# Performance work log

Measured on AMD Instinct MI355X. Metric: run time of the kernel, lower is better.

Reference implementation:

```python
import jax, jax.numpy as jnp
import numpy as np
from functools import partial

VOCAB, EMB, HID, B, T, K = 30000, 256, 512, 128, 256, 12
START, STOP = 10, 11


def lstm_scan(xs, mask, W_ih, W_hh, b_ih, b_hh, h0, c0):
    """xs: [T,B,E], mask: [T,B] bool. PyTorch gate order i,f,g,o. Masked steps carry state (packed-seq semantics)."""
    def step(carry, inp):
        h, c = carry
        x_t, m_t = inp
        gates = x_t @ W_ih.T + h @ W_hh.T + (b_ih + b_hh)  # [B,4H]
        i, f, g, o = jnp.split(gates, 4, axis=-1)
        c_new = jax.nn.sigmoid(f) * c + jax.nn.sigmoid(i) * jnp.tanh(g)
        h_new = jax.nn.sigmoid(o) * jnp.tanh(c_new)
        m = m_t[:, None]
        h = jnp.where(m, h_new, h)
        c = jnp.where(m, c_new, c)
        return (h, c), h
    _, hs = jax.lax.scan(step, (h0, c0), (xs, mask))
    return hs  # [T,B,H]


def crf_log_partition(emissions, mask, trans):
    """emissions: [T,B,K], mask: [T,B]. Vectorized log-sum-exp forward algorithm."""
    b, k = emissions.shape[1], emissions.shape[2]
    alpha0 = jnp.full((b, k), -10000.0, emissions.dtype).at[:, START].set(0.0)
    def step(alpha, inp):
        emit_t, m_t = inp
        # alpha_new[b,j] = logsumexp_i(alpha[b,i] + trans[j,i]) + emit[b,j]
        scores = alpha[:, None, :] + trans[None, :, :]  # [B,Knext,Kprev]
        alpha_new = jax.nn.logsumexp(scores, axis=-1) + emit_t
        return jnp.where(m_t[:, None], alpha_new, alpha), None
    alpha, _ = jax.lax.scan(step, alpha0, (emissions, mask))
    return jax.nn.logsumexp(alpha + trans[STOP][None, :], axis=-1)  # [B]


def crf_gold_score(emissions_bt, tags, lengths, trans):
    """emissions_bt: [B,T,K]. Gold path score with <start> prepended and <stop> transition."""
    b, t = tags.shape
    tags_ext = jnp.concatenate([jnp.full((b, 1), START, tags.dtype), tags], axis=1)  # [B,T+1]
    prev, nxt = tags_ext[:, :-1], tags_ext[:, 1:]  # [B,T]
    trans_s = trans[nxt, prev]  # [B,T]
    emit_s = jnp.take_along_axis(emissions_bt, nxt[:, :, None], axis=2)[:, :, 0]  # [B,T]
    valid = jnp.arange(t)[None, :] < lengths[:, None]  # [B,T]
    score = jnp.sum(jnp.where(valid, trans_s + emit_s, 0.0), axis=1)
    last_tag = jnp.take_along_axis(tags, (lengths - 1)[:, None], axis=1)[:, 0]
    return score + trans[STOP, last_tag]


def setup_inputs() -> dict:
    key = jax.random.key(0)
    ks = jax.random.split(key, 16)
    s = 0.1
    x = jax.random.randint(ks[0], (B, T), 0, VOCAB)
    lengths = jax.random.randint(ks[1], (B,), 1, T + 1)
    tags = jax.random.randint(ks[2], (B, T), 0, K - 2)  # real labels only
    embedding = jax.random.normal(ks[3], (VOCAB, EMB), jnp.float32) * s
    W_ih_f = jax.random.normal(ks[4], (4 * HID, EMB), jnp.float32) * s
    W_hh_f = jax.random.normal(ks[5], (4 * HID, HID), jnp.float32) * s
    b_ih_f = jax.random.normal(ks[6], (4 * HID,), jnp.float32) * s
    b_hh_f = jax.random.normal(ks[7], (4 * HID,), jnp.float32) * s
    W_ih_b = jax.random.normal(ks[8], (4 * HID, EMB), jnp.float32) * s
    W_hh_b = jax.random.normal(ks[9], (4 * HID, HID), jnp.float32) * s
    b_ih_b = jax.random.normal(ks[10], (4 * HID,), jnp.float32) * s
    b_hh_b = jax.random.normal(ks[11], (4 * HID,), jnp.float32) * s
    fc_W = jax.random.normal(ks[12], (K, 2 * HID), jnp.float32) * s
    fc_b = jnp.zeros((K,), jnp.float32)
    trans = jax.random.normal(ks[13], (K, K), jnp.float32) * s
    trans = trans.at[START, :].set(-10000.0).at[:, STOP].set(-10000.0)
    h0 = jax.random.normal(ks[14], (2, B, HID), jnp.float32) * s
    c0 = jax.random.normal(ks[15], (2, B, HID), jnp.float32) * s
    return dict(x=x, lengths=lengths, tags=tags, embedding=embedding,
                W_ih_f=W_ih_f, W_hh_f=W_hh_f, b_ih_f=b_ih_f, b_hh_f=b_hh_f,
                W_ih_b=W_ih_b, W_hh_b=W_hh_b, b_ih_b=b_ih_b, b_hh_b=b_hh_b,
                fc_W=fc_W, fc_b=fc_b, trans=trans, h0=h0, c0=c0)


def reference(x, lengths, tags, embedding, W_ih_f, W_hh_f, b_ih_f, b_hh_f,
              W_ih_b, W_hh_b, b_ih_b, b_hh_b, fc_W, fc_b, trans, h0, c0):
    # neg_log_likelihood: BiLSTM emission feats -> CRF logZ - gold score. Dropout = eval (identity).
    emb = embedding[x]                 # [B,T,E]
    xs = emb.transpose(1, 0, 2)        # [T,B,E] time-major
    t = xs.shape[0]
    mask = jnp.arange(t)[:, None] < lengths[None, :]  # [T,B]
    hs_f = lstm_scan(xs, mask, W_ih_f, W_hh_f, b_ih_f, b_hh_f, h0[0], c0[0])
    hs_b = lstm_scan(xs[::-1], mask[::-1], W_ih_b, W_hh_b, b_ih_b, b_hh_b, h0[1], c0[1])[::-1]
    out = jnp.concatenate([hs_f, hs_b], axis=-1)      # [T,B,2H]
    emissions = out @ fc_W.T + fc_b                    # [T,B,K]
    log_z = crf_log_partition(emissions, mask, trans)  # [B]
    gold = crf_gold_score(emissions.transpose(1, 0, 2), tags, lengths, trans)  # [B]
    return log_z - gold  # per-sentence NLL, [B]
```

## Files before the change

kernel.cpp:

```cpp
#include <hip/hip_runtime.h>
#include <hip/hip_bf16.h>

#define TT 256
#define BB 128
#define EMBD 256
#define HID 512
#define KTAG 12
#define START_TAG 10
#define STOP_TAG 11
#define SMEM_BYTES 148608

typedef __attribute__((ext_vector_type(8))) short short8;
typedef __attribute__((ext_vector_type(4))) float f32x4;

__device__ __forceinline__ unsigned short f2bf(float f) {
    union { float f; unsigned int u; } v; v.f = f;
    unsigned int r = v.u + 0x7fffu + ((v.u >> 16) & 1u);
    return (unsigned short)(r >> 16);
}
__device__ __forceinline__ float fsig(float x) {
    return __fdividef(1.0f, 1.0f + __expf(-x));
}
__device__ __forceinline__ float ftanh(float x) {
    return 2.0f * __fdividef(1.0f, 1.0f + __expf(-2.0f * x)) - 1.0f;
}
__device__ __forceinline__ void gll16(const void* g, void* l) {
    __builtin_amdgcn_global_load_lds((const __attribute__((address_space(1))) void*)g,
                                     (__attribute__((address_space(3))) void*)l, 16, 0, 0);
}
__device__ __forceinline__ void pack8(const float* src, unsigned short* dst) {
    float4 v0 = *(const float4*)src;
    float4 v1 = *(const float4*)(src + 4);
    unsigned short tmp[8];
    tmp[0] = f2bf(v0.x); tmp[1] = f2bf(v0.y); tmp[2] = f2bf(v0.z); tmp[3] = f2bf(v0.w);
    tmp[4] = f2bf(v1.x); tmp[5] = f2bf(v1.y); tmp[6] = f2bf(v1.z); tmp[7] = f2bf(v1.w);
    *(uint4*)dst = *(const uint4*)tmp;
}

__global__ void prologue(const int* __restrict__ x, const float* __restrict__ emb,
                         const float* __restrict__ Wihf, const float* __restrict__ Whhf,
                         const float* __restrict__ Wihb, const float* __restrict__ Whhb,
                         const float* __restrict__ h0,
                         const float* __restrict__ bihf, const float* __restrict__ bhhf,
                         const float* __restrict__ bihb, const float* __restrict__ bhhb,
                         const float* __restrict__ fcW,
                         unsigned short* __restrict__ xs, unsigned short* __restrict__ Wr,
                         unsigned short* __restrict__ h0buf, float* __restrict__ bias2,
                         unsigned short* __restrict__ fcWr, unsigned int* __restrict__ ctrl)
{
    int blk = blockIdx.x;
    int tid = threadIdx.x;
    if (blk < 4096) {
        int i = blk * 256 + tid;
        int chk = i & 31;
        int row = i >> 5;
        int b = row & (BB - 1);
        int t = row >> 7;
        pack8(emb + (size_t)x[b * TT + t] * EMBD + chk * 8, xs + (size_t)row * EMBD + chk * 8);
    } else if (blk < 5632) {
        int i = (blk - 4096) * 256 + tid;
        int c8 = i % 96;
        int r2 = i / 96;
        int nr = r2 & 2047;
        int dir = r2 >> 11;
        int utile = nr >> 6;
        int r6 = nr & 63;
        int wm = r6 >> 4;
        int rr = r6 & 15;
        int ul = rr >> 2, g = rr & 3;
        int orow = g * HID + utile * 16 + wm * 4 + ul;
        int k0 = c8 * 8;
        const float* Wih = dir ? Wihb : Wihf;
        const float* Whh = dir ? Whhb : Whhf;
        const float* src = (k0 < EMBD) ? (Wih + (size_t)orow * EMBD + k0)
                                       : (Whh + (size_t)orow * HID + (k0 - EMBD));
        pack8(src, Wr + ((size_t)dir * 2048 + nr) * 768 + k0);
    } else {
        int i = (blk - 5632) * 256 + tid;
        if (i < 2 * BB * HID) h0buf[i] = f2bf(h0[i]);
        if (i < 2 * 2048) {
            int dir = i >> 11, j = i & 2047;
            bias2[i] = dir ? (bihb[j] + bhhb[j]) : (bihf[j] + bhhf[j]);
        }
        if (i < 16 * 1024) {
            int tag = i >> 10, k = i & 1023;
            fcWr[i] = f2bf(tag < KTAG ? fcW[tag * 1024 + k] : 0.0f);
        }
        if (i < 512) ctrl[i] = 0u;
    }
}

__launch_bounds__(256, 1)
__global__ void lstm_persistent(
    const unsigned short* __restrict__ xs, const unsigned short* __restrict__ Wr,
    const float* __restrict__ bias2, const int* __restrict__ lengths,
    const unsigned short* __restrict__ h0buf, const float* __restrict__ c0,
    unsigned short* __restrict__ hsf, unsigned short* __restrict__ hsb,
    unsigned int* __restrict__ ctrl)
{
    extern __shared__ char smem[];
    unsigned short* Wlds = (unsigned short*)smem;
    unsigned short* Abuf = (unsigned short*)(smem + 98304);
    unsigned short* hrep = (unsigned short*)(smem + 147456);

    const int blk = blockIdx.x;
    const int grp = blk & 7;
    const int dir = grp >> 2;
    const int btile = grp & 3;
    const int utile = blk >> 3;
    const int bg0 = btile * 32;

    const int tid = threadIdx.x;
    const int w = tid >> 6;
    const int l = tid & 63;
    const int l15 = l & 15, l16 = l >> 4;

    unsigned int* gflags = ctrl + 64 + grp * 32;

    unsigned short* hs = dir ? hsb : hsf;
    unsigned int* hs_u32 = (unsigned int*)hs;

    {
        const unsigned short* src0 =
            Wr + ((size_t)(dir * 2048 + utile * 64) + (w * 16 + l15)) * 768 + l16 * 8;
        #pragma unroll
        for (int ks = 0; ks < 24; ks++)
            gll16(src0 + ks * 32, Wlds + (w * 24 + ks) * 512);
    }

    const int u = utile * 16 + w * 4 + l16;
    const int bA = bg0 + l15, bB = bg0 + 16 + l15;
    const int lenA = lengths[bA], lenB = lengths[bB];
    float cA = c0[((size_t)dir * BB + bA) * HID + u];
    float cB = c0[((size_t)dir * BB + bB) * HID + u];
    float bias_r[4];
    #pragma unroll
    for (int g = 0; g < 4; g++) bias_r[g] = bias2[dir * 2048 + g * 512 + u];

    for (int s = 0; s < TT; s++) {
        const int t = dir ? (TT - 1 - s) : s;

        {
            int mm = w & 1, ksb = (w >> 1) * 4;
            const unsigned short* asrc =
                xs + ((size_t)t * BB + (bg0 + mm * 16 + l15)) * EMBD + l16 * 8;
            #pragma unroll
            for (int q = 0; q < 4; q++)
                gll16(asrc + (ksb + q) * 32, Abuf + (mm * 24 + ksb + q) * 512);
        }
        __syncthreads();

        f32x4 aA0 = {0.f,0.f,0.f,0.f}, aA1 = {0.f,0.f,0.f,0.f};
        f32x4 aB0 = {0.f,0.f,0.f,0.f}, aB1 = {0.f,0.f,0.f,0.f};
        auto mstep = [&](int ks, f32x4& xA, f32x4& xB) {
            short8 a  = *(const short8*)(Wlds + ((w * 24 + ks) << 9) + (l << 3));
            short8 b0 = *(const short8*)(Abuf + (ks << 9) + (l << 3));
            short8 b1 = *(const short8*)(Abuf + ((24 + ks) << 9) + (l << 3));
            xA = __builtin_amdgcn_mfma_f32_16x16x32_bf16(a, b0, xA, 0, 0, 0);
            xB = __builtin_amdgcn_mfma_f32_16x16x32_bf16(a, b1, xB, 0, 0, 0);
        };
        #pragma unroll
        for (int ks = 0; ks < 8; ks += 2) { mstep(ks, aA0, aB0); mstep(ks + 1, aA1, aB1); }

        if (s > 0) {
            if (tid < 64) {
                unsigned tgt = (unsigned)s;
                unsigned fidx = (unsigned)tid & 31u;
                while (true) {
                    unsigned v = __hip_atomic_load(&gflags[fidx], __ATOMIC_RELAXED,
                                                   __HIP_MEMORY_SCOPE_AGENT);
                    if (__all(v >= tgt)) break;
                }
            }
            __syncthreads();
        }
        const unsigned short* hsrc = (s == 0)
            ? (h0buf + (size_t)dir * BB * HID)
            : (hs + (size_t)(dir ? (t + 1) : (t - 1)) * BB * HID);

        {
            int mm = w & 1, ksb = 8 + (w >> 1) * 8;
            const unsigned short* asrcH = hsrc + (size_t)(bg0 + mm * 16 + l15) * HID + l16 * 8;
            #pragma unroll
            for (int q = 0; q < 8; q++)
                gll16(asrcH + ((ksb + q) * 32 - 256), Abuf + (mm * 24 + ksb + q) * 512);
        }
        __syncthreads();

        #pragma unroll
        for (int ks = 8; ks < 24; ks += 2) { mstep(ks, aA0, aB0); mstep(ks + 1, aA1, aB1); }
        f32x4 accA = aA0 + aA1;
        f32x4 accB = aB0 + aB1;

        {
            const int ksn = 8 + (u >> 5), kin = u & 31;
            const int baseA = ksn * 512 + ((kin >> 3) * 16 + l15) * 8 + (kin & 7);
            const int baseB = (24 + ksn) * 512 + ((kin >> 3) * 16 + l15) * 8 + (kin & 7);
            float giA = accA[0] + bias_r[0], gfA = accA[1] + bias_r[1];
            float ggA = accA[2] + bias_r[2], goA = accA[3] + bias_r[3];
            float cnA = fsig(gfA) * cA + fsig(giA) * ftanh(ggA);
            float hnA = fsig(goA) * ftanh(cnA);
            float giB = accB[0] + bias_r[0], gfB = accB[1] + bias_r[1];
            float ggB = accB[2] + bias_r[2], goB = accB[3] + bias_r[3];
            float cnB = fsig(gfB) * cB + fsig(giB) * ftanh(ggB);
            float hnB = fsig(goB) * ftanh(cnB);
            bool mA = t < lenA, mB = t < lenB;
            unsigned short hvA = mA ? f2bf(hnA) : Abuf[baseA];
            unsigned short hvB = mB ? f2bf(hnB) : Abuf[baseB];
            cA = mA ? cnA : cA;
            cB = mB ? cnB : cB;
            hrep[l15 * 18 + w * 4 + l16]        = hvA;
            hrep[(16 + l15) * 18 + w * 4 + l16] = hvB;
        }
        __syncthreads();

        {
            int bl = tid >> 3, up = tid & 7;
            unsigned v0 = hrep[bl * 18 + up * 2];
            unsigned v1 = hrep[bl * 18 + up * 2 + 1];
            unsigned pk = v0 | (v1 << 16);
            size_t widx = (((size_t)t * BB + (bg0 + bl)) * HID + utile * 16 + up * 2) >> 1;
            __hip_atomic_store(hs_u32 + widx, pk, __ATOMIC_RELAXED, __HIP_MEMORY_SCOPE_AGENT);
        }
        __syncthreads();

        if (tid == 0)
            __hip_atomic_store(&gflags[utile], (unsigned)(s + 1), __ATOMIC_RELAXED,
                               __HIP_MEMORY_SCOPE_AGENT);
    }
}

__global__ void emissions_mfma(const unsigned short* __restrict__ hsf,
                               const unsigned short* __restrict__ hsb,
                               const unsigned short* __restrict__ fcWr,
                               const float* __restrict__ fcb, float* __restrict__ emis)
{
    int wid = (blockIdx.x * blockDim.x + threadIdx.x) >> 6;
    int l = threadIdx.x & 63;
    int l15 = l & 15, l16 = l >> 4;
    int rowbase = wid * 16;
    f32x4 acc0 = {0.f,0.f,0.f,0.f}, acc1 = {0.f,0.f,0.f,0.f};
    auto estep = [&](const unsigned short* hsp, int ks, f32x4& acc) {
        short8 av = *(const short8*)(hsp + (size_t)(rowbase + l15) * HID + (ks & 15) * 32 + l16 * 8);
        short8 bv = *(const short8*)(fcWr + l15 * 1024 + ks * 32 + l16 * 8);
        acc = __builtin_amdgcn_mfma_f32_16x16x32_bf16(av, bv, acc, 0, 0, 0);
    };
    #pragma unroll
    for (int ks = 0; ks < 16; ks += 2) { estep(hsf, ks, acc0); estep(hsf, ks + 1, acc1); }
    #pragma unroll
    for (int ks = 16; ks < 32; ks += 2) { estep(hsb, ks, acc0); estep(hsb, ks + 1, acc1); }
    f32x4 acc = acc0 + acc1;
    float bval = fcb[l15 < KTAG ? l15 : 0];
    if (l15 < KTAG) {
        #pragma unroll
        for (int r = 0; r < 4; r++)
            emis[(size_t)(rowbase + 4 * l16 + r) * KTAG + l15] = acc[r] + bval;
    }
}

__global__ void crf_gold(const float* __restrict__ emis, const int* __restrict__ lengths,
                         const int* __restrict__ tags, const float* __restrict__ trans,
                         float* __restrict__ out)
{
    __shared__ float s_logz, s_gold;
    int b = blockIdx.x;
    int tid = threadIdx.x;
    int len = lengths[b];
    if (tid < 64) {
        int lane = tid;
        float trow[KTAG];
        #pragma unroll
        for (int j = 0; j < KTAG; j++)
            trow[j] = (lane < KTAG) ? trans[lane * KTAG + j] : -1e30f;
        float alpha = (lane == START_TAG) ? 0.0f : -10000.0f;
        float e_cur = (lane < KTAG) ? emis[(size_t)b * KTAG + lane] : 0.0f;
        for (int t = 0; t < len; t++) {
            int tn = (t + 1 < TT) ? t + 1 : t;
            float e_next = (lane < KTAG) ? emis[(size_t)(tn * BB + b) * KTAG + lane] : 0.0f;
            float sc[KTAG];
            #pragma unroll
            for (int j = 0; j < KTAG; j++) sc[j] = __shfl(alpha, j, 64) + trow[j];
            float m = sc[0];
            #pragma unroll
            for (int j = 1; j < KTAG; j++) m = fmaxf(m, sc[j]);
            float ssum = 0.0f;
            #pragma unroll
            for (int j = 0; j < KTAG; j++) ssum += __expf(sc[j] - m);
            float anew = m + __logf(ssum) + e_cur;
            alpha = (lane < KTAG) ? anew : alpha;
            e_cur = e_next;
        }
        float v = (lane < KTAG) ? (alpha + trans[STOP_TAG * KTAG + lane]) : -1e30f;
        float m = v;
        #pragma unroll
        for (int off = 1; off < 16; off <<= 1) m = fmaxf(m, __shfl_xor(m, off, 64));
        float e = __expf(v - m);
        #pragma unroll
        for (int off = 1; off < 16; off <<= 1) e += __shfl_xor(e, off, 64);
        if (lane == 0) s_logz = m + __logf(e);
    } else {
        int l2 = tid - 64;
        float part = 0.0f;
        #pragma unroll
        for (int q = 0; q < 4; q++) {
            int t = l2 + q * 64;
            if (t < len) {
                int nxt = tags[b * TT + t];
                int prev = t ? tags[b * TT + t - 1] : START_TAG;
                part += trans[nxt * KTAG + prev] + emis[(size_t)(t * BB + b) * KTAG + nxt];
            }
        }
        #pragma unroll
        for (int off = 1; off < 64; off <<= 1) part += __shfl_xor(part, off, 64);
        if (l2 == 0) s_gold = part + trans[STOP_TAG * KTAG + tags[b * TT + len - 1]];
    }
    __syncthreads();
    if (tid == 0) out[b] = s_logz - s_gold;
}

extern "C" void kernel_launch(void* const* d_in, const int* in_sizes, int n_in,
                              void* d_out, int out_size, void* d_ws, size_t ws_size,
                              hipStream_t stream)
{
    (void)in_sizes; (void)n_in; (void)out_size; (void)ws_size;
    const int*   x     = (const int*)d_in[0];
    const int*   lens  = (const int*)d_in[1];
    const int*   tags  = (const int*)d_in[2];
    const float* emb   = (const float*)d_in[3];
    const float* Wihf  = (const float*)d_in[4];
    const float* Whhf  = (const float*)d_in[5];
    const float* bihf  = (const float*)d_in[6];
    const float* bhhf  = (const float*)d_in[7];
    const float* Wihb  = (const float*)d_in[8];
    const float* Whhb  = (const float*)d_in[9];
    const float* bihb  = (const float*)d_in[10];
    const float* bhhb  = (const float*)d_in[11];
    const float* fcW   = (const float*)d_in[12];
    const float* fcb   = (const float*)d_in[13];
    const float* trans = (const float*)d_in[14];
    const float* h0    = (const float*)d_in[15];
    const float* c0    = (const float*)d_in[16];
    float* out = (float*)d_out;

    char* ws = (char*)d_ws;
    size_t off = 0;
    auto alloc = [&](size_t bytes) {
        void* p = ws + off;
        off += (bytes + 255) & ~(size_t)255;
        return p;
    };
    unsigned short* xs    = (unsigned short*)alloc((size_t)TT * BB * EMBD * 2);
    unsigned short* Wr    = (unsigned short*)alloc((size_t)2 * 2048 * 768 * 2);
    float*          bias2 = (float*)alloc((size_t)2 * 2048 * 4);
    unsigned short* h0buf = (unsigned short*)alloc((size_t)2 * BB * HID * 2);
    unsigned short* hsf   = (unsigned short*)alloc((size_t)TT * BB * HID * 2);
    unsigned short* hsb   = (unsigned short*)alloc((size_t)TT * BB * HID * 2);
    float*          emis  = (float*)alloc((size_t)TT * BB * KTAG * 4);
    unsigned short* fcWr  = (unsigned short*)alloc((size_t)16 * 1024 * 2);
    unsigned int*   ctrl  = (unsigned int*)alloc((size_t)512 * 4);

    prologue<<<6144, 256, 0, stream>>>(x, emb, Wihf, Whhf, Wihb, Whhb, h0,
                                       bihf, bhhf, bihb, bhhb, fcW,
                                       xs, Wr, h0buf, bias2, fcWr, ctrl);

    hipFuncSetAttribute(reinterpret_cast<const void*>(lstm_persistent),
                        hipFuncAttributeMaxDynamicSharedMemorySize, SMEM_BYTES);
    {
        const unsigned short* p_xs = xs; const unsigned short* p_Wr = Wr;
        const float* p_bias2 = bias2; const int* p_lens = lens;
        const unsigned short* p_h0 = h0buf; const float* p_c0 = c0;
        unsigned short* p_hsf = hsf; unsigned short* p_hsb = hsb;
        unsigned int* p_ctrl = ctrl;
        void* args[9] = { &p_xs, &p_Wr, &p_bias2, &p_lens, &p_h0, &p_c0,
                          &p_hsf, &p_hsb, &p_ctrl };
        hipError_t e = hipLaunchCooperativeKernel(
            reinterpret_cast<const void*>(lstm_persistent),
            dim3(256), dim3(256), args, (unsigned)SMEM_BYTES, stream);
        if (e != hipSuccess) {
            lstm_persistent<<<256, 256, SMEM_BYTES, stream>>>(
                xs, Wr, bias2, lens, h0buf, c0, hsf, hsb, ctrl);
        }
    }

    emissions_mfma<<<512, 256, 0, stream>>>(hsf, hsb, fcWr, fcb, emis);
    crf_gold<<<BB, 128, 0, stream>>>(emis, lens, tags, trans, out);
}
```

Before: 1.110 ms.

## Detect same-XCD block groups and use XCD-scoped flag sync

At startup each block records its XCC id, and a group-wide handshake checks whether all 32 blocks of its recurrence group sit on the same XCD. If they do, the per-step hidden-state stores and flag signalling use plain or sc0-only (shorter cache scope) loads and stores instead of agent-scope atomics. This is meant to cut the inter-block synchronisation latency paid on every timestep. It relies on the hardware block-to-XCD placement for the mode to trigger, and it adds a startup barrier plus a fallback to agent-scope loads after a spin limit.

```diff
diff --git a/kernel.cpp b/kernel.cpp
--- a/kernel.cpp
+++ b/kernel.cpp
@@ -86,7 +86,7 @@
             int tag = i >> 10, k = i & 1023;
             fcWr[i] = f2bf(tag < KTAG ? fcW[tag * 1024 + k] : 0.0f);
         }
-        if (i < 512) ctrl[i] = 0u;
+        if (i < 1024) ctrl[i] = 0u;
     }
 }
 
@@ -102,6 +102,7 @@
     unsigned short* Wlds = (unsigned short*)smem;
     unsigned short* Abuf = (unsigned short*)(smem + 98304);
     unsigned short* hrep = (unsigned short*)(smem + 147456);
+    __shared__ unsigned mode_sh;
 
     const int blk = blockIdx.x;
     const int grp = blk & 7;
@@ -115,7 +116,9 @@
     const int l = tid & 63;
     const int l15 = l & 15, l16 = l >> 4;
 
+    unsigned int* hcnt   = ctrl + 16 + grp;
     unsigned int* gflags = ctrl + 64 + grp * 32;
+    unsigned int* xcdmap = ctrl + 320 + grp * 32;
 
     unsigned short* hs = dir ? hsb : hsf;
     unsigned int* hs_u32 = (unsigned int*)hs;
@@ -127,6 +130,28 @@
         for (int ks = 0; ks < 24; ks++)
             gll16(src0 + ks * 32, Wlds + (w * 24 + ks) * 512);
     }
+
+    {
+        unsigned xcc;
+        asm volatile("s_getreg_b32 %0, hwreg(HW_REG_XCC_ID, 0, 32)" : "=s"(xcc));
+        xcc &= 7u;
+        if (tid == 0) {
+            __hip_atomic_store(&xcdmap[utile], xcc + 1u, __ATOMIC_RELAXED,
+                               __HIP_MEMORY_SCOPE_AGENT);
+            __hip_atomic_fetch_add(hcnt, 1u, __ATOMIC_ACQ_REL, __HIP_MEMORY_SCOPE_AGENT);
+            while (__hip_atomic_load(hcnt, __ATOMIC_ACQUIRE, __HIP_MEMORY_SCOPE_AGENT) < 32u)
+                __builtin_amdgcn_s_sleep(2);
+        }
+        __syncthreads();
+        if (tid < 64) {
+            unsigned v = __hip_atomic_load(&xcdmap[tid & 31u], __ATOMIC_RELAXED,
+                                           __HIP_MEMORY_SCOPE_AGENT);
+            unsigned same = __all(v == (xcc + 1u)) ? 1u : 0u;
+            if (tid == 0) mode_sh = same;
+        }
+        __syncthreads();
+    }
+    const bool modeA = (mode_sh != 0u);
 
     const int u = utile * 16 + w * 4 + l16;
     const int bA = bg0 + l15, bB = bg0 + 16 + l15;
@@ -165,11 +190,28 @@
         if (s > 0) {
             if (tid < 64) {
                 unsigned tgt = (unsigned)s;
-                unsigned fidx = (unsigned)tid & 31u;
-                while (true) {
-                    unsigned v = __hip_atomic_load(&gflags[fidx], __ATOMIC_RELAXED,
-                                                   __HIP_MEMORY_SCOPE_AGENT);
-                    if (__all(v >= tgt)) break;
+                const unsigned int* fp = gflags + (tid & 31u);
+                if (modeA) {
+                    int spin = 0;
+                    while (true) {
+                        unsigned v;
+                        if (spin < (1 << 20)) {
+                            asm volatile("global_load_dword %0, %1, off sc0\n\t"
+                                         "s_waitcnt vmcnt(0)"
+                                         : "=v"(v) : "v"(fp) : "memory");
+                        } else {
+                            v = __hip_atomic_load(fp, __ATOMIC_RELAXED,
+                                                  __HIP_MEMORY_SCOPE_AGENT);
+                        }
+                        if (__all(v >= tgt)) break;
+                        ++spin;
+                    }
+                } else {
+                    while (true) {
+                        unsigned v = __hip_atomic_load(fp, __ATOMIC_RELAXED,
+                                                       __HIP_MEMORY_SCOPE_AGENT);
+                        if (__all(v >= tgt)) break;
+                    }
                 }
             }
             __syncthreads();
@@ -220,13 +262,26 @@
             unsigned v1 = hrep[bl * 18 + up * 2 + 1];
             unsigned pk = v0 | (v1 << 16);
             size_t widx = (((size_t)t * BB + (bg0 + bl)) * HID + utile * 16 + up * 2) >> 1;
-            __hip_atomic_store(hs_u32 + widx, pk, __ATOMIC_RELAXED, __HIP_MEMORY_SCOPE_AGENT);
-        }
-        __syncthreads();
-
-        if (tid == 0)
-            __hip_atomic_store(&gflags[utile], (unsigned)(s + 1), __ATOMIC_RELAXED,
-                               __HIP_MEMORY_SCOPE_AGENT);
+            if (modeA) {
+                hs_u32[widx] = pk;
+            } else {
+                __hip_atomic_store(hs_u32 + widx, pk, __ATOMIC_RELAXED,
+                                   __HIP_MEMORY_SCOPE_AGENT);
+            }
+        }
+        __syncthreads();
+
+        if (tid == 0) {
+            if (modeA) {
+                unsigned int* fp = gflags + utile;
+                unsigned val = (unsigned)(s + 1);
+                asm volatile("global_store_dword %0, %1, off sc0"
+                             :: "v"(fp), "v"(val) : "memory");
+            } else {
+                __hip_atomic_store(&gflags[utile], (unsigned)(s + 1), __ATOMIC_RELAXED,
+                                   __HIP_MEMORY_SCOPE_AGENT);
+            }
+        }
     }
 }
 
@@ -357,7 +412,7 @@
     unsigned short* hsb   = (unsigned short*)alloc((size_t)TT * BB * HID * 2);
     float*          emis  = (float*)alloc((size_t)TT * BB * KTAG * 4);
     unsigned short* fcWr  = (unsigned short*)alloc((size_t)16 * 1024 * 2);
-    unsigned int*   ctrl  = (unsigned int*)alloc((size_t)512 * 4);
+    unsigned int*   ctrl  = (unsigned int*)alloc((size_t)1024 * 4);
 
     prologue<<<6144, 256, 0, stream>>>(x, emb, Wihf, Whhf, Wihb, Whhb, h0,
                                        bihf, bhhf, bihb, bhhb, fcW,
```

Measured after the change: 2.839 ms. +155.8%, slower.

## Use per-wave step flags, prefetch next x tile, and split h-load wait

Applied to the files above, without the earlier changes.

Each wave now publishes its own progress flag, so the block-wide barrier before the flag store goes away. Pollers read pairs of flags with 64-bit loads and keep one load in flight while they spin. The x-tile load for the next step is issued at the end of the current step, and the h-tile wait is split into two vmcnt waits so the first half of the MFMAs can start early. Bias is folded into the accumulator initialisation. The cost is more flags to poll and reliance on hand-placed waitcnt and barrier ordering, which could hide a race if the counts are wrong.

```diff
diff --git a/kernel.cpp b/kernel.cpp
--- a/kernel.cpp
+++ b/kernel.cpp
@@ -36,6 +36,11 @@
     tmp[4] = f2bf(v1.x); tmp[5] = f2bf(v1.y); tmp[6] = f2bf(v1.z); tmp[7] = f2bf(v1.w);
     *(uint4*)dst = *(const uint4*)tmp;
 }
+
+#define SCHED_FENCE() __builtin_amdgcn_sched_barrier(0)
+#define WAIT_VM4() do { asm volatile("s_waitcnt vmcnt(4)" ::: "memory"); SCHED_FENCE(); } while (0)
+#define WAIT_VM0() do { asm volatile("s_waitcnt vmcnt(0)" ::: "memory"); SCHED_FENCE(); } while (0)
+#define BARRIER_RAW() do { __builtin_amdgcn_s_barrier(); SCHED_FENCE(); } while (0)
 
 __global__ void prologue(const int* __restrict__ x, const float* __restrict__ emb,
                          const float* __restrict__ Wihf, const float* __restrict__ Whhf,
@@ -86,7 +91,7 @@
             int tag = i >> 10, k = i & 1023;
             fcWr[i] = f2bf(tag < KTAG ? fcW[tag * 1024 + k] : 0.0f);
         }
-        if (i < 512) ctrl[i] = 0u;
+        if (i < 2048) ctrl[i] = 0u;
     }
 }
 
@@ -115,7 +120,8 @@
     const int l = tid & 63;
     const int l15 = l & 15, l16 = l >> 4;
 
-    unsigned int* gflags = ctrl + 64 + grp * 32;
+    unsigned int* wflags = ctrl + 64 + grp * 128;
+    unsigned int* myflag = wflags + utile * 4 + w;
 
     unsigned short* hs = dir ? hsb : hsf;
     unsigned int* hs_u32 = (unsigned int*)hs;
@@ -126,6 +132,15 @@
         #pragma unroll
         for (int ks = 0; ks < 24; ks++)
             gll16(src0 + ks * 32, Wlds + (w * 24 + ks) * 512);
+    }
+    {
+        int mm = w & 1, ksb = (w >> 1) * 4;
+        const int t0 = dir ? (TT - 1) : 0;
+        const unsigned short* asrc =
+            xs + ((size_t)t0 * BB + (bg0 + mm * 16 + l15)) * EMBD + l16 * 8;
+        #pragma unroll
+        for (int q = 0; q < 4; q++)
+            gll16(asrc + (ksb + q) * 32, Abuf + (mm * 24 + ksb + q) * 512);
     }
 
     const int u = utile * 16 + w * 4 + l16;
@@ -140,18 +155,11 @@
     for (int s = 0; s < TT; s++) {
         const int t = dir ? (TT - 1 - s) : s;
 
-        {
-            int mm = w & 1, ksb = (w >> 1) * 4;
-            const unsigned short* asrc =
-                xs + ((size_t)t * BB + (bg0 + mm * 16 + l15)) * EMBD + l16 * 8;
-            #pragma unroll
-            for (int q = 0; q < 4; q++)
-                gll16(asrc + (ksb + q) * 32, Abuf + (mm * 24 + ksb + q) * 512);
-        }
         __syncthreads();
 
-        f32x4 aA0 = {0.f,0.f,0.f,0.f}, aA1 = {0.f,0.f,0.f,0.f};
-        f32x4 aB0 = {0.f,0.f,0.f,0.f}, aB1 = {0.f,0.f,0.f,0.f};
+        f32x4 aA0 = {bias_r[0], bias_r[1], bias_r[2], bias_r[3]};
+        f32x4 aB0 = {bias_r[0], bias_r[1], bias_r[2], bias_r[3]};
+        f32x4 aA1 = {0.f,0.f,0.f,0.f}, aB1 = {0.f,0.f,0.f,0.f};
         auto mstep = [&](int ks, f32x4& xA, f32x4& xB) {
             short8 a  = *(const short8*)(Wlds + ((w * 24 + ks) << 9) + (l << 3));
             short8 b0 = *(const short8*)(Abuf + (ks << 9) + (l << 3));
@@ -165,11 +173,17 @@
         if (s > 0) {
             if (tid < 64) {
                 unsigned tgt = (unsigned)s;
-                unsigned fidx = (unsigned)tid & 31u;
+                const unsigned long long* fp =
+                    (const unsigned long long*)(wflags + 2 * (tid & 63));
+                unsigned long long v0 = __hip_atomic_load(fp, __ATOMIC_RELAXED,
+                                                          __HIP_MEMORY_SCOPE_AGENT);
+                unsigned long long v1 = __hip_atomic_load(fp, __ATOMIC_RELAXED,
+                                                          __HIP_MEMORY_SCOPE_AGENT);
                 while (true) {
-                    unsigned v = __hip_atomic_load(&gflags[fidx], __ATOMIC_RELAXED,
-                                                   __HIP_MEMORY_SCOPE_AGENT);
-                    if (__all(v >= tgt)) break;
+                    bool ok = ((unsigned)v0 >= tgt) && ((unsigned)(v0 >> 32) >= tgt);
+                    if (__all(ok)) break;
+                    v0 = v1;
+                    v1 = __hip_atomic_load(fp, __ATOMIC_RELAXED, __HIP_MEMORY_SCOPE_AGENT);
                 }
             }
             __syncthreads();
@@ -185,10 +199,15 @@
             for (int q = 0; q < 8; q++)
                 gll16(asrcH + ((ksb + q) * 32 - 256), Abuf + (mm * 24 + ksb + q) * 512);
         }
-        __syncthreads();
-
-        #pragma unroll
-        for (int ks = 8; ks < 24; ks += 2) { mstep(ks, aA0, aB0); mstep(ks + 1, aA1, aB1); }
+        SCHED_FENCE();
+        WAIT_VM4();
+        BARRIER_RAW();
+        #pragma unroll
+        for (int q = 0; q < 4; q++) { mstep(8 + q, aA0, aB0); mstep(16 + q, aA1, aB1); }
+        WAIT_VM0();
+        BARRIER_RAW();
+        #pragma unroll
+        for (int q = 0; q < 4; q++) { mstep(12 + q, aA0, aB0); mstep(20 + q, aA1, aB1); }
         f32x4 accA = aA0 + aA1;
         f32x4 accB = aB0 + aB1;
 
@@ -196,14 +215,10 @@
             const int ksn = 8 + (u >> 5), kin = u & 31;
             const int baseA = ksn * 512 + ((kin >> 3) * 16 + l15) * 8 + (kin & 7);
             const int baseB = (24 + ksn) * 512 + ((kin >> 3) * 16 + l15) * 8 + (kin & 7);
-            float giA = accA[0] + bias_r[0], gfA = accA[1] + bias_r[1];
-            float ggA = accA[2] + bias_r[2], goA = accA[3] + bias_r[3];
-            float cnA = fsig(gfA) * cA + fsig(giA) * ftanh(ggA);
-            float hnA = fsig(goA) * ftanh(cnA);
-            float giB = accB[0] + bias_r[0], gfB = accB[1] + bias_r[1];
-            float ggB = accB[2] + bias_r[2], goB = accB[3] + bias_r[3];
-            float cnB = fsig(gfB) * cB + fsig(giB) * ftanh(ggB);
-            float hnB = fsig(goB) * ftanh(cnB);
+            float cnA = fsig(accA[1]) * cA + fsig(accA[0]) * ftanh(accA[2]);
+            float hnA = fsig(accA[3]) * ftanh(cnA);
+            float cnB = fsig(accB[1]) * cB + fsig(accB[0]) * ftanh(accB[2]);
+            float hnB = fsig(accB[3]) * ftanh(cnB);
             bool mA = t < lenA, mB = t < lenB;
             unsigned short hvA = mA ? f2bf(hnA) : Abuf[baseA];
             unsigned short hvB = mB ? f2bf(hnB) : Abuf[baseB];
@@ -222,11 +237,21 @@
             size_t widx = (((size_t)t * BB + (bg0 + bl)) * HID + utile * 16 + up * 2) >> 1;
             __hip_atomic_store(hs_u32 + widx, pk, __ATOMIC_RELAXED, __HIP_MEMORY_SCOPE_AGENT);
         }
-        __syncthreads();
-
-        if (tid == 0)
-            __hip_atomic_store(&gflags[utile], (unsigned)(s + 1), __ATOMIC_RELAXED,
-                               __HIP_MEMORY_SCOPE_AGENT);
+        SCHED_FENCE();
+        if (s < TT - 1) {
+            const int tn = dir ? (TT - 2 - s) : (s + 1);
+            int mm = w & 1, ksb = (w >> 1) * 4;
+            const unsigned short* asrc =
+                xs + ((size_t)tn * BB + (bg0 + mm * 16 + l15)) * EMBD + l16 * 8;
+            #pragma unroll
+            for (int q = 0; q < 4; q++)
+                gll16(asrc + (ksb + q) * 32, Abuf + (mm * 24 + ksb + q) * 512);
+            SCHED_FENCE();
+            WAIT_VM4();
+            if (l == 0)
+                __hip_atomic_store(myflag, (unsigned)(s + 1), __ATOMIC_RELAXED,
+                                   __HIP_MEMORY_SCOPE_AGENT);
+        }
     }
 }
 
@@ -357,7 +382,7 @@
     unsigned short* hsb   = (unsigned short*)alloc((size_t)TT * BB * HID * 2);
     float*          emis  = (float*)alloc((size_t)TT * BB * KTAG * 4);
     unsigned short* fcWr  = (unsigned short*)alloc((size_t)16 * 1024 * 2);
-    unsigned int*   ctrl  = (unsigned int*)alloc((size_t)512 * 4);
+    unsigned int*   ctrl  = (unsigned int*)alloc((size_t)2048 * 4);
 
     prologue<<<6144, 256, 0, stream>>>(x, emb, Wihf, Whhf, Wihb, Whhb, h0,
                                        bihf, bhhf, bihb, bhhb, fcW,
```

Result: faster. 1.071 ms (-3.5%).

## Exchange LSTM hidden state via tagged 64-bit words instead of flag barriers

Applied to the files above, without the earlier changes.

Each block now publishes its new hidden-state slice as 64-bit words that pair the bf16 data with a step tag, written into a double-buffered exchange array. Consumers poll those words directly and scatter them into LDS. This removes the separate flag store/poll round trip and the staging syncs through the shared `hrep` buffer. The next step's embedding tile is prefetched right after the gate math, and the bias is folded into the accumulator init. The recurrence loop also stops at the maximum length in each batch tile, so fully padded timesteps are skipped; the hidden states for those steps are no longer written. The cost is more polling traffic (32 atomic loads per thread per step) and a larger exchange buffer to zero in the prologue.

```diff
diff --git a/kernel.cpp b/kernel.cpp
--- a/kernel.cpp
+++ b/kernel.cpp
@@ -8,10 +8,11 @@
 #define KTAG 12
 #define START_TAG 10
 #define STOP_TAG 11
-#define SMEM_BYTES 148608
+#define SMEM_BYTES 147456
 
 typedef __attribute__((ext_vector_type(8))) short short8;
 typedef __attribute__((ext_vector_type(4))) float f32x4;
+typedef unsigned long long ull;
 
 __device__ __forceinline__ unsigned short f2bf(float f) {
     union { float f; unsigned int u; } v; v.f = f;
@@ -46,7 +47,7 @@
                          const float* __restrict__ fcW,
                          unsigned short* __restrict__ xs, unsigned short* __restrict__ Wr,
                          unsigned short* __restrict__ h0buf, float* __restrict__ bias2,
-                         unsigned short* __restrict__ fcWr, unsigned int* __restrict__ ctrl)
+                         unsigned short* __restrict__ fcWr, ull* __restrict__ hx)
 {
     int blk = blockIdx.x;
     int tid = threadIdx.x;
@@ -75,7 +76,7 @@
         const float* src = (k0 < EMBD) ? (Wih + (size_t)orow * EMBD + k0)
                                        : (Whh + (size_t)orow * HID + (k0 - EMBD));
         pack8(src, Wr + ((size_t)dir * 2048 + nr) * 768 + k0);
-    } else {
+    } else if (blk < 6144) {
         int i = (blk - 5632) * 256 + tid;
         if (i < 2 * BB * HID) h0buf[i] = f2bf(h0[i]);
         if (i < 2 * 2048) {
@@ -86,7 +87,9 @@
             int tag = i >> 10, k = i & 1023;
             fcWr[i] = f2bf(tag < KTAG ? fcW[tag * 1024 + k] : 0.0f);
         }
-        if (i < 512) ctrl[i] = 0u;
+    } else {
+        int i = (blk - 6144) * 256 + tid;
+        hx[i] = 0ull;
     }
 }
 
@@ -96,12 +99,13 @@
     const float* __restrict__ bias2, const int* __restrict__ lengths,
     const unsigned short* __restrict__ h0buf, const float* __restrict__ c0,
     unsigned short* __restrict__ hsf, unsigned short* __restrict__ hsb,
-    unsigned int* __restrict__ ctrl)
+    ull* __restrict__ hx)
 {
     extern __shared__ char smem[];
     unsigned short* Wlds = (unsigned short*)smem;
     unsigned short* Abuf = (unsigned short*)(smem + 98304);
-    unsigned short* hrep = (unsigned short*)(smem + 147456);
+    char* AbufB = (char*)Abuf;
+    __shared__ int s_ml;
 
     const int blk = blockIdx.x;
     const int grp = blk & 7;
@@ -115,10 +119,19 @@
     const int l = tid & 63;
     const int l15 = l & 15, l16 = l >> 4;
 
-    unsigned int* gflags = ctrl + 64 + grp * 32;
-
     unsigned short* hs = dir ? hsb : hsf;
     unsigned int* hs_u32 = (unsigned int*)hs;
+
+    {
+        int v = (tid < 32) ? lengths[bg0 + tid] : 0;
+        if (tid < 64) {
+            #pragma unroll
+            for (int off = 32; off >= 1; off >>= 1) v = max(v, __shfl_xor(v, off, 64));
+            if (tid == 0) s_ml = v;
+        }
+    }
+    __syncthreads();
+    const int TTs = s_ml;
 
     {
         const unsigned short* src0 =
@@ -126,6 +139,15 @@
         #pragma unroll
         for (int ks = 0; ks < 24; ks++)
             gll16(src0 + ks * 32, Wlds + (w * 24 + ks) * 512);
+    }
+    {
+        int mm = w & 1, ksb = (w >> 1) * 4;
+        const int t0 = dir ? (TTs - 1) : 0;
+        const unsigned short* asrc =
+            xs + ((size_t)t0 * BB + (bg0 + mm * 16 + l15)) * EMBD + l16 * 8;
+        #pragma unroll
+        for (int q = 0; q < 4; q++)
+            gll16(asrc + (ksb + q) * 32, Abuf + (mm * 24 + ksb + q) * 512);
     }
 
     const int u = utile * 16 + w * 4 + l16;
@@ -137,21 +159,28 @@
     #pragma unroll
     for (int g = 0; g < 4; g++) bias_r[g] = bias2[dir * 2048 + g * 512 + u];
 
-    for (int s = 0; s < TT; s++) {
-        const int t = dir ? (TT - 1 - s) : s;
-
-        {
-            int mm = w & 1, ksb = (w >> 1) * 4;
-            const unsigned short* asrc =
-                xs + ((size_t)t * BB + (bg0 + mm * 16 + l15)) * EMBD + l16 * 8;
-            #pragma unroll
-            for (int q = 0; q < 4; q++)
-                gll16(asrc + (ksb + q) * 32, Abuf + (mm * 24 + ksb + q) * 512);
-        }
+    const int b_local = tid >> 3, q = tid & 7;
+    const int mm_c = b_local >> 4, b15_c = b_local & 15;
+    const int C0 = 2 * ((mm_c * 24 + 8) * 512 + (q >> 2) * 128 + b15_c * 8 + 2 * (q & 3));
+
+    for (int k = 0; k < TTs; k++) {
+        const int t = dir ? (TTs - 1 - k) : k;
+
         __syncthreads();
 
-        f32x4 aA0 = {0.f,0.f,0.f,0.f}, aA1 = {0.f,0.f,0.f,0.f};
-        f32x4 aB0 = {0.f,0.f,0.f,0.f}, aB1 = {0.f,0.f,0.f,0.f};
+        ull pv[32];
+        const ull* pbase = hx + (((size_t)dir * 2 + ((k - 1) & 1)) * 128 + bg0 + b_local) * 256 + q;
+        if (k > 0) {
+            #pragma unroll
+            for (int j = 0; j < 32; j++)
+                pv[j] = __hip_atomic_load(pbase + 8 * j, __ATOMIC_RELAXED,
+                                          __HIP_MEMORY_SCOPE_AGENT);
+            __builtin_amdgcn_sched_barrier(0);
+        }
+
+        f32x4 aA0 = {bias_r[0], bias_r[1], bias_r[2], bias_r[3]};
+        f32x4 aB0 = {bias_r[0], bias_r[1], bias_r[2], bias_r[3]};
+        f32x4 aA1 = {0.f,0.f,0.f,0.f}, aB1 = {0.f,0.f,0.f,0.f};
         auto mstep = [&](int ks, f32x4& xA, f32x4& xB) {
             short8 a  = *(const short8*)(Wlds + ((w * 24 + ks) << 9) + (l << 3));
             short8 b0 = *(const short8*)(Abuf + (ks << 9) + (l << 3));
@@ -162,71 +191,88 @@
         #pragma unroll
         for (int ks = 0; ks < 8; ks += 2) { mstep(ks, aA0, aB0); mstep(ks + 1, aA1, aB1); }
 
-        if (s > 0) {
-            if (tid < 64) {
-                unsigned tgt = (unsigned)s;
-                unsigned fidx = (unsigned)tid & 31u;
-                while (true) {
-                    unsigned v = __hip_atomic_load(&gflags[fidx], __ATOMIC_RELAXED,
-                                                   __HIP_MEMORY_SCOPE_AGENT);
-                    if (__all(v >= tgt)) break;
+        if (k == 0) {
+            int mm = w & 1, ksb = 8 + (w >> 1) * 8;
+            const unsigned short* asrcH =
+                h0buf + (size_t)dir * BB * HID + (size_t)(bg0 + mm * 16 + l15) * HID + l16 * 8;
+            #pragma unroll
+            for (int p = 0; p < 8; p++)
+                gll16(asrcH + ((ksb + p) * 32 - 256), Abuf + (mm * 24 + ksb + p) * 512);
+            __syncthreads();
+        } else {
+            unsigned need = 0xffffffffu;
+            const unsigned tagw = (unsigned)k;
+            #pragma unroll
+            for (int j = 0; j < 32; j++) {
+                if ((unsigned)(pv[j] >> 32) == tagw) {
+                    need &= ~(1u << j);
+                    *(unsigned*)(AbufB + C0 + (j >> 1) * 1024 + (j & 1) * 512) = (unsigned)pv[j];
+                }
+            }
+            while (need) {
+                #pragma unroll
+                for (int j = 0; j < 32; j++) {
+                    if (need & (1u << j)) {
+                        ull v = __hip_atomic_load(pbase + 8 * j, __ATOMIC_RELAXED,
+                                                  __HIP_MEMORY_SCOPE_AGENT);
+                        if ((unsigned)(v >> 32) == tagw) {
+                            need &= ~(1u << j);
+                            *(unsigned*)(AbufB + C0 + (j >> 1) * 1024 + (j & 1) * 512) = (unsigned)v;
+                        }
+                    }
                 }
             }
             __syncthreads();
         }
-        const unsigned short* hsrc = (s == 0)
-            ? (h0buf + (size_t)dir * BB * HID)
-            : (hs + (size_t)(dir ? (t + 1) : (t - 1)) * BB * HID);
-
-        {
-            int mm = w & 1, ksb = 8 + (w >> 1) * 8;
-            const unsigned short* asrcH = hsrc + (size_t)(bg0 + mm * 16 + l15) * HID + l16 * 8;
-            #pragma unroll
-            for (int q = 0; q < 8; q++)
-                gll16(asrcH + ((ksb + q) * 32 - 256), Abuf + (mm * 24 + ksb + q) * 512);
-        }
-        __syncthreads();
 
         #pragma unroll
         for (int ks = 8; ks < 24; ks += 2) { mstep(ks, aA0, aB0); mstep(ks + 1, aA1, aB1); }
         f32x4 accA = aA0 + aA1;
         f32x4 accB = aB0 + aB1;
 
+        unsigned short hvA, hvB;
         {
             const int ksn = 8 + (u >> 5), kin = u & 31;
             const int baseA = ksn * 512 + ((kin >> 3) * 16 + l15) * 8 + (kin & 7);
             const int baseB = (24 + ksn) * 512 + ((kin >> 3) * 16 + l15) * 8 + (kin & 7);
-            float giA = accA[0] + bias_r[0], gfA = accA[1] + bias_r[1];
-            float ggA = accA[2] + bias_r[2], goA = accA[3] + bias_r[3];
-            float cnA = fsig(gfA) * cA + fsig(giA) * ftanh(ggA);
-            float hnA = fsig(goA) * ftanh(cnA);
-            float giB = accB[0] + bias_r[0], gfB = accB[1] + bias_r[1];
-            float ggB = accB[2] + bias_r[2], goB = accB[3] + bias_r[3];
-            float cnB = fsig(gfB) * cB + fsig(giB) * ftanh(ggB);
-            float hnB = fsig(goB) * ftanh(cnB);
+            float cnA = fsig(accA[1]) * cA + fsig(accA[0]) * ftanh(accA[2]);
+            float hnA = fsig(accA[3]) * ftanh(cnA);
+            float cnB = fsig(accB[1]) * cB + fsig(accB[0]) * ftanh(accB[2]);
+            float hnB = fsig(accB[3]) * ftanh(cnB);
             bool mA = t < lenA, mB = t < lenB;
-            unsigned short hvA = mA ? f2bf(hnA) : Abuf[baseA];
-            unsigned short hvB = mB ? f2bf(hnB) : Abuf[baseB];
+            hvA = mA ? f2bf(hnA) : Abuf[baseA];
+            hvB = mB ? f2bf(hnB) : Abuf[baseB];
             cA = mA ? cnA : cA;
             cB = mB ? cnB : cB;
-            hrep[l15 * 18 + w * 4 + l16]        = hvA;
-            hrep[(16 + l15) * 18 + w * 4 + l16] = hvB;
-        }
-        __syncthreads();
+        }
 
         {
-            int bl = tid >> 3, up = tid & 7;
-            unsigned v0 = hrep[bl * 18 + up * 2];
-            unsigned v1 = hrep[bl * 18 + up * 2 + 1];
-            unsigned pk = v0 | (v1 << 16);
-            size_t widx = (((size_t)t * BB + (bg0 + bl)) * HID + utile * 16 + up * 2) >> 1;
-            __hip_atomic_store(hs_u32 + widx, pk, __ATOMIC_RELAXED, __HIP_MEMORY_SCOPE_AGENT);
-        }
-        __syncthreads();
-
-        if (tid == 0)
-            __hip_atomic_store(&gflags[utile], (unsigned)(s + 1), __ATOMIC_RELAXED,
-                               __HIP_MEMORY_SCOPE_AGENT);
+            int sA = __shfl_xor((int)hvA, 16, 64);
+            int sB = __shfl_xor((int)hvB, 16, 64);
+            if ((l16 & 1) == 0) {
+                unsigned pkA = (unsigned)hvA | ((unsigned)sA << 16);
+                unsigned pkB = (unsigned)hvB | ((unsigned)sB << 16);
+                int wd = utile * 8 + w * 2 + (l16 >> 1);
+                ull tv = ((ull)(unsigned)(k + 1)) << 32;
+                size_t hxbase = ((size_t)dir * 2 + (k & 1)) * 128;
+                __hip_atomic_store(hx + (hxbase + bA) * 256 + wd, (ull)pkA | tv,
+                                   __ATOMIC_RELAXED, __HIP_MEMORY_SCOPE_AGENT);
+                __hip_atomic_store(hx + (hxbase + bB) * 256 + wd, (ull)pkB | tv,
+                                   __ATOMIC_RELAXED, __HIP_MEMORY_SCOPE_AGENT);
+                hs_u32[((size_t)t * BB + bA) * 256 + wd] = pkA;
+                hs_u32[((size_t)t * BB + bB) * 256 + wd] = pkB;
+            }
+        }
+
+        if (k < TTs - 1) {
+            const int tn = dir ? (TTs - 2 - k) : (k + 1);
+            int mm = w & 1, ksb = (w >> 1) * 4;
+            const unsigned short* asrc =
+                xs + ((size_t)tn * BB + (bg0 + mm * 16 + l15)) * EMBD + l16 * 8;
+            #pragma unroll
+            for (int p = 0; p < 4; p++)
+                gll16(asrc + (ksb + p) * 32, Abuf + (mm * 24 + ksb + p) * 512);
+        }
     }
 }
 
@@ -302,8 +348,8 @@
         int l2 = tid - 64;
         float part = 0.0f;
         #pragma unroll
-        for (int q = 0; q < 4; q++) {
-            int t = l2 + q * 64;
+        for (int qq = 0; qq < 4; qq++) {
+            int t = l2 + qq * 64;
             if (t < len) {
                 int nxt = tags[b * TT + t];
                 int prev = t ? tags[b * TT + t - 1] : START_TAG;
@@ -357,11 +403,11 @@
     unsigned short* hsb   = (unsigned short*)alloc((size_t)TT * BB * HID * 2);
     float*          emis  = (float*)alloc((size_t)TT * BB * KTAG * 4);
     unsigned short* fcWr  = (unsigned short*)alloc((size_t)16 * 1024 * 2);
-    unsigned int*   ctrl  = (unsigned int*)alloc((size_t)512 * 4);
-
-    prologue<<<6144, 256, 0, stream>>>(x, emb, Wihf, Whhf, Wihb, Whhb, h0,
+    ull*            hx    = (ull*)alloc((size_t)2 * 2 * BB * (HID / 2) * 8);
+
+    prologue<<<7168, 256, 0, stream>>>(x, emb, Wihf, Whhf, Wihb, Whhb, h0,
                                        bihf, bhhf, bihb, bhhb, fcW,
-                                       xs, Wr, h0buf, bias2, fcWr, ctrl);
+                                       xs, Wr, h0buf, bias2, fcWr, hx);
 
     hipFuncSetAttribute(reinterpret_cast<const void*>(lstm_persistent),
                         hipFuncAttributeMaxDynamicSharedMemorySize, SMEM_BYTES);
@@ -370,15 +416,15 @@
         const float* p_bias2 = bias2; const int* p_lens = lens;
         const unsigned short* p_h0 = h0buf; const float* p_c0 = c0;
         unsigned short* p_hsf = hsf; unsigned short* p_hsb = hsb;
-        unsigned int* p_ctrl = ctrl;
+        ull* p_hx = hx;
         void* args[9] = { &p_xs, &p_Wr, &p_bias2, &p_lens, &p_h0, &p_c0,
-                          &p_hsf, &p_hsb, &p_ctrl };
+                          &p_hsf, &p_hsb, &p_hx };
         hipError_t e = hipLaunchCooperativeKernel(
             reinterpret_cast<const void*>(lstm_persistent),
             dim3(256), dim3(256), args, (unsigned)SMEM_BYTES, stream);
         if (e != hipSuccess) {
             lstm_persistent<<<256, 256, SMEM_BYTES, stream>>>(
-                xs, Wr, bias2, lens, h0buf, c0, hsf, hsb, ctrl);
+                xs, Wr, bias2, lens, h0buf, c0, hsf, hsb, hx);
         }
     }
 
```

New measurement: 3.446 ms. 210% more time.
